# Optimization experiments

Measured on AMD Instinct MI355X. Metric: run time of the kernel, lower is better.

The kernel has to match this reference:

```python
import jax, jax.numpy as jnp
import numpy as np

H = 2048      # hidden_dim
OUT = 8       # output_dim
DICT = 50000  # dict_len (DND capacity)
FDIM = 6      # function_dim
RDIM = 1      # rule_dim
IN = FDIM + RDIM + OUT + 1  # input_dim = 16
NG = 5        # N_GATES
EPS = 1e-8


def setup_inputs() -> dict:
    key = jax.random.key(0)
    ks = jax.random.split(key, 16)
    f = lambda i, shape, s=1.0: jax.random.normal(ks[i], shape, jnp.float32) * s
    return {
        "x_t": f(0, (1, IN)),
        "h": f(1, (1, 1, H), 0.1),
        "c": f(2, (1, 1, H), 0.1),
        "W_i2h": f(3, ((NG + 1) * H, IN), 0.05),
        "b_i2h": jnp.zeros(((NG + 1) * H,), jnp.float32),
        "W_h2h": f(4, ((NG + 1) * H, H), 0.02),
        "b_h2h": jnp.zeros(((NG + 1) * H,), jnp.float32),
        "f_keys": f(5, (DICT, FDIM)),
        "f_vals": f(6, (DICT, H), 0.1),
        "r_keys": f(7, (DICT, RDIM)),
        "r_vals": f(8, (DICT, H), 0.1),
        "W_ih": f(9, (H, H), 0.02),
        "b_ih": jnp.zeros((H,), jnp.float32),
        "W_actor": f(10, (OUT, H), 0.02),
        "b_actor": jnp.zeros((OUT,), jnp.float32),
        "W_critic": f(11, (1, H), 0.02),
        "b_critic": jnp.zeros((1,), jnp.float32),
        "write_idx": 12345,
    }


def _dnd_read(q, keys, vals):
    # cosine similarity between query q [d] and all keys [N, d], softmax policy,
    # weighted sum over stored values [N, H] -> [H]
    qn = q / (jnp.linalg.norm(q) + EPS)
    kn = keys / (jnp.linalg.norm(keys, axis=1, keepdims=True) + EPS)
    sim = kn @ qn                      # [N]
    w = jax.nn.softmax(sim)            # [N]
    return w @ vals                    # [H]


def reference(x_t, h, c, W_i2h, b_i2h, W_h2h, b_h2h,
              f_keys, f_vals, r_keys, r_vals,
              W_ih, b_ih, W_actor, b_actor, W_critic, b_critic,
              write_idx):
    h2 = h.reshape(1, H)
    c2 = c.reshape(1, H)

    # fused gate preactivations: [1, 6H]
    preact = x_t @ W_i2h.T + b_i2h + h2 @ W_h2h.T + b_h2h
    gates = jax.nn.sigmoid(preact[:, :NG * H])
    f_t = gates[:, 0 * H:1 * H]
    i_t = gates[:, 1 * H:2 * H]
    o_t = gates[:, 2 * H:3 * H]
    fun_t = gates[:, 3 * H:4 * H]
    rul_t = gates[:, 4 * H:5 * H]
    c_new = jnp.tanh(preact[:, NG * H:])

    c_t = f_t * c2 + i_t * c_new

    # DND content-addressable reads (cosine sim + softmax over memory slots)
    q_f = x_t[0, :FDIM]
    q_r = x_t[0, FDIM:FDIM + RDIM]
    memfun_t = jnp.tanh(_dnd_read(q_f, f_keys, f_vals))  # [H]
    memrul_t = jnp.tanh(_dnd_read(q_r, r_keys, r_vals))  # [H]

    c_t = c_t + fun_t * memfun_t + rul_t * memrul_t
    h_t = o_t * jnp.tanh(c_t)

    # memory write (no-grad in original): function half / rule half of c_t
    c_ft = jax.lax.stop_gradient(c_t[0].at[H // 2:].set(0.0))
    c_rt = jax.lax.stop_gradient(c_t[0].at[:H // 2].set(0.0))
    new_f_keys = f_keys.at[write_idx].set(q_f)
    new_f_vals = f_vals.at[write_idx].set(c_ft)
    new_r_keys = r_keys.at[write_idx].set(q_r)
    new_r_vals = r_vals.at[write_idx].set(c_rt)

    # A2C head: shared relu layer, actor softmax, critic scalar
    ha = jax.nn.relu(h_t @ W_ih.T + b_ih)
    pi_a_t = jax.nn.softmax(ha @ W_actor.T + b_actor, axis=-1)  # [1, OUT]
    v_t = ha @ W_critic.T + b_critic                            # [1, 1]

    h_out = h_t.reshape(1, 1, H)
    c_out = c_t.reshape(1, 1, H)
    return (pi_a_t, v_t, h_out, c_out,
            new_f_keys, new_f_vals, new_r_keys, new_r_vals)
```

## Files before the change

### kernel.cpp

```cpp
#include <hip/hip_runtime.h>
#include <math.h>

#define H        2048
#define HD       12288
#define DICT     50000
#define FDIM     6
#define RDIM     1
#define IN_DIM   16
#define EPS_F    1e-8f

#define OFF_PI   ((size_t)0)
#define OFF_V    ((size_t)8)
#define OFF_H    ((size_t)9)
#define OFF_C    ((size_t)2057)
#define OFF_FK   ((size_t)4105)
#define OFF_FV   ((size_t)304105)
#define OFF_RK   ((size_t)102704105)
#define OFF_RV   ((size_t)102754105)

#define R_CHUNK      125
#define NBLK_DICT    (DICT / R_CHUNK)
#define NBLK_VALS    (2 * NBLK_DICT)
#define NBLK_PREACT  (HD / 8)
#define NBLK_TOTAL   (NBLK_VALS + NBLK_PREACT)

typedef float f4v __attribute__((ext_vector_type(4)));

__device__ __forceinline__ float sigf(float v) { return 1.0f / (1.0f + expf(-v)); }

__global__ void k_zero(float* __restrict__ p, int n) {
    int i = blockIdx.x * 256 + threadIdx.x;
    if (i < n) p[i] = 0.0f;
}

__global__ __launch_bounds__(512) void k_mega(
    const float* __restrict__ f_keys, const float* __restrict__ r_keys,
    const float* __restrict__ f_vals, const float* __restrict__ r_vals,
    const float* __restrict__ x,
    const float* __restrict__ W_h2h, const float* __restrict__ W_i2h,
    const float* __restrict__ b_h2h, const float* __restrict__ b_i2h,
    const float* __restrict__ h,
    float* __restrict__ out_fv, float* __restrict__ out_rv,
    float* __restrict__ out_fk, float* __restrict__ out_rk,
    float* __restrict__ memfun, float* __restrict__ memrul,
    float* __restrict__ sums, float* __restrict__ preact)
{
    const int b   = blockIdx.x;
    const int tid = threadIdx.x;

    if (b >= NBLK_VALS) {
        const int row  = (b - NBLK_VALS) * 8 + (tid >> 6);
        const int lane = tid & 63;
        const float4* Wv = (const float4*)(W_h2h + (size_t)row * H);
        const float4* hv = (const float4*)h;
        float acc = 0.0f;
#pragma unroll
        for (int k = 0; k < 8; ++k) {
            float4 w4 = Wv[lane + (k << 6)];
            float4 h4 = hv[lane + (k << 6)];
            acc += w4.x * h4.x + w4.y * h4.y + w4.z * h4.z + w4.w * h4.w;
        }
        if (lane < IN_DIM) acc += W_i2h[(size_t)row * IN_DIM + lane] * x[lane];
#pragma unroll
        for (int off = 32; off > 0; off >>= 1) acc += __shfl_down(acc, off);
        if (lane == 0) preact[row] = acc + b_h2h[row] + b_i2h[row];
        return;
    }

    __shared__ float wl[R_CHUNK];
    const int  dict = (b >= NBLK_DICT) ? 1 : 0;
    const int  row0 = (dict ? b - NBLK_DICT : b) * R_CHUNK;

    const float* vals = dict ? r_vals : f_vals;
    float*       outv = dict ? out_rv : out_fv;
    float*       mem  = dict ? memrul : memfun;

    if (!dict) {
        for (int i = tid; i < R_CHUNK * FDIM; i += 512)
            out_fk[(size_t)row0 * FDIM + i] = f_keys[(size_t)row0 * FDIM + i];
    } else if (tid < R_CHUNK) {
        out_rk[row0 + tid] = r_keys[row0 + tid];
    }

    if (tid < R_CHUNK) {
        const int row = row0 + tid;
        float e;
        if (!dict) {
            float qn[FDIM]; float qs = 0.0f;
#pragma unroll
            for (int d = 0; d < FDIM; ++d) { float q = x[d]; qn[d] = q; qs += q * q; }
            const float qi = 1.0f / (sqrtf(qs) + EPS_F);
            float ks = 0.0f, dot = 0.0f;
#pragma unroll
            for (int d = 0; d < FDIM; ++d) {
                float kv = f_keys[(size_t)row * FDIM + d];
                ks += kv * kv; dot += kv * qn[d];
            }
            e = expf((dot * qi) / (sqrtf(ks) + EPS_F));
        } else {
            float q  = x[FDIM];
            float kv = r_keys[row];
            e = expf((kv * (q / (fabsf(q) + EPS_F))) / (fabsf(kv) + EPS_F));
        }
        wl[tid] = e;
    }
    __syncthreads();
    if (tid == 0) {
        float s = 0.0f;
        for (int i = 0; i < R_CHUNK; ++i) s += wl[i];
        atomicAdd(&sums[dict], s);
    }

    const f4v* vv = (const f4v*)vals;
    float a0 = 0.f, a1 = 0.f, a2 = 0.f, a3 = 0.f;
    size_t base = (size_t)row0 * 512 + tid;
    for (int i0 = 0; i0 < R_CHUNK; i0 += 5) {
        f4v v0 = __builtin_nontemporal_load(&vv[base]);
        f4v v1 = __builtin_nontemporal_load(&vv[base +  512]);
        f4v v2 = __builtin_nontemporal_load(&vv[base + 1024]);
        f4v v3 = __builtin_nontemporal_load(&vv[base + 1536]);
        f4v v4 = __builtin_nontemporal_load(&vv[base + 2048]);
        const float w0 = wl[i0], w1 = wl[i0+1], w2 = wl[i0+2], w3 = wl[i0+3], w4 = wl[i0+4];
        a0 += w0*v0.x + w1*v1.x + w2*v2.x + w3*v3.x + w4*v4.x;
        a1 += w0*v0.y + w1*v1.y + w2*v2.y + w3*v3.y + w4*v4.y;
        a2 += w0*v0.z + w1*v1.z + w2*v2.z + w3*v3.z + w4*v4.z;
        a3 += w0*v0.w + w1*v1.w + w2*v2.w + w3*v3.w + w4*v4.w;
        float* o0 = outv + (base        ) * 4;
        float* o1 = outv + (base +  512 ) * 4;
        float* o2 = outv + (base + 1024 ) * 4;
        float* o3 = outv + (base + 1536 ) * 4;
        float* o4 = outv + (base + 2048 ) * 4;
        __builtin_nontemporal_store(v0.x, o0+0); __builtin_nontemporal_store(v0.y, o0+1);
        __builtin_nontemporal_store(v0.z, o0+2); __builtin_nontemporal_store(v0.w, o0+3);
        __builtin_nontemporal_store(v1.x, o1+0); __builtin_nontemporal_store(v1.y, o1+1);
        __builtin_nontemporal_store(v1.z, o1+2); __builtin_nontemporal_store(v1.w, o1+3);
        __builtin_nontemporal_store(v2.x, o2+0); __builtin_nontemporal_store(v2.y, o2+1);
        __builtin_nontemporal_store(v2.z, o2+2); __builtin_nontemporal_store(v2.w, o2+3);
        __builtin_nontemporal_store(v3.x, o3+0); __builtin_nontemporal_store(v3.y, o3+1);
        __builtin_nontemporal_store(v3.z, o3+2); __builtin_nontemporal_store(v3.w, o3+3);
        __builtin_nontemporal_store(v4.x, o4+0); __builtin_nontemporal_store(v4.y, o4+1);
        __builtin_nontemporal_store(v4.z, o4+2); __builtin_nontemporal_store(v4.w, o4+3);
        base += 5 * 512;
    }
    const int c = tid * 4;
    atomicAdd(&mem[c + 0], a0);
    atomicAdd(&mem[c + 1], a1);
    atomicAdd(&mem[c + 2], a2);
    atomicAdd(&mem[c + 3], a3);
}

__global__ __launch_bounds__(256) void k_combine(
    const float* __restrict__ preact, const float* __restrict__ c_in,
    const float* __restrict__ memfun, const float* __restrict__ memrul,
    const float* __restrict__ sums,
    const float* __restrict__ x, const int* __restrict__ widx_p,
    float* __restrict__ out, float* __restrict__ ht_ws)
{
    const int j = blockIdx.x * 256 + threadIdx.x;
    if (j >= H) return;
    const int widx = *widx_p;
    const float invf = 1.0f / sums[0];
    const float invr = 1.0f / sums[1];

    float f_t   = sigf(preact[0 * H + j]);
    float i_t   = sigf(preact[1 * H + j]);
    float o_t   = sigf(preact[2 * H + j]);
    float fun_t = sigf(preact[3 * H + j]);
    float rul_t = sigf(preact[4 * H + j]);
    float c_new = tanhf(preact[5 * H + j]);

    float ct = f_t * c_in[j] + i_t * c_new
             + fun_t * tanhf(memfun[j] * invf) + rul_t * tanhf(memrul[j] * invr);
    float ht = o_t * tanhf(ct);

    out[OFF_H + j] = ht;
    out[OFF_C + j] = ct;
    ht_ws[j] = ht;

    out[OFF_FV + (size_t)widx * H + j] = (j < H / 2) ? ct : 0.0f;
    out[OFF_RV + (size_t)widx * H + j] = (j < H / 2) ? 0.0f : ct;
    if (j < FDIM)  out[OFF_FK + (size_t)widx * FDIM + j] = x[j];
    if (j == FDIM) out[OFF_RK + (size_t)widx] = x[FDIM];
}

__global__ __launch_bounds__(256) void k_hidden(
    const float* __restrict__ W_ih, const float* __restrict__ b_ih,
    const float* __restrict__ ht, float* __restrict__ ha)
{
    int gid  = blockIdx.x * blockDim.x + threadIdx.x;
    int row  = gid >> 6;
    int lane = threadIdx.x & 63;
    if (row >= H) return;
    const float4* Wv = (const float4*)(W_ih + (size_t)row * H);
    const float4* hv = (const float4*)ht;
    float acc = 0.0f;
#pragma unroll
    for (int k = 0; k < 8; ++k) {
        float4 w4 = Wv[lane + (k << 6)];
        float4 h4 = hv[lane + (k << 6)];
        acc += w4.x * h4.x + w4.y * h4.y + w4.z * h4.z + w4.w * h4.w;
    }
#pragma unroll
    for (int off = 32; off > 0; off >>= 1) acc += __shfl_down(acc, off);
    if (lane == 0) ha[row] = fmaxf(acc + b_ih[row], 0.0f);
}

__global__ __launch_bounds__(256) void k_heads(
    const float* __restrict__ W_actor, const float* __restrict__ b_actor,
    const float* __restrict__ W_critic, const float* __restrict__ b_critic,
    const float* __restrict__ ha, float* __restrict__ out)
{
    __shared__ float red[4];
    __shared__ float logits[9];
    const int tid = threadIdx.x;

    for (int o = 0; o < 9; ++o) {
        const float* row = (o < 8) ? (W_actor + (size_t)o * H) : W_critic;
        float acc = 0.0f;
        for (int k = tid; k < H; k += 256) acc += row[k] * ha[k];
#pragma unroll
        for (int off = 32; off > 0; off >>= 1) acc += __shfl_down(acc, off);
        if ((tid & 63) == 0) red[tid >> 6] = acc;
        __syncthreads();
        if (tid == 0)
            logits[o] = red[0] + red[1] + red[2] + red[3] + ((o < 8) ? b_actor[o] : b_critic[0]);
        __syncthreads();
    }
    if (tid == 0) {
        float m = logits[0];
        for (int o = 1; o < 8; ++o) m = fmaxf(m, logits[o]);
        float e[8], s = 0.0f;
        for (int o = 0; o < 8; ++o) { e[o] = expf(logits[o] - m); s += e[o]; }
        for (int o = 0; o < 8; ++o) out[OFF_PI + o] = e[o] / s;
        out[OFF_V] = logits[8];
    }
}

extern "C" void kernel_launch(void* const* d_in, const int* in_sizes, int n_in,
                              void* d_out, int out_size, void* d_ws, size_t ws_size,
                              hipStream_t stream)
{
    const float* x        = (const float*)d_in[0];
    const float* h        = (const float*)d_in[1];
    const float* c        = (const float*)d_in[2];
    const float* W_i2h    = (const float*)d_in[3];
    const float* b_i2h    = (const float*)d_in[4];
    const float* W_h2h    = (const float*)d_in[5];
    const float* b_h2h    = (const float*)d_in[6];
    const float* f_keys   = (const float*)d_in[7];
    const float* f_vals   = (const float*)d_in[8];
    const float* r_keys   = (const float*)d_in[9];
    const float* r_vals   = (const float*)d_in[10];
    const float* W_ih     = (const float*)d_in[11];
    const float* b_ih     = (const float*)d_in[12];
    const float* W_actor  = (const float*)d_in[13];
    const float* b_actor  = (const float*)d_in[14];
    const float* W_critic = (const float*)d_in[15];
    const float* b_critic = (const float*)d_in[16];
    const int*   widx     = (const int*)d_in[17];

    float* out = (float*)d_out;
    float* ws  = (float*)d_ws;

    float* preact = ws;
    float* memfun = ws + 12288;
    float* memrul = ws + 14336;
    float* sums   = ws + 16384;
    float* ht_ws  = ws + 16388;
    float* ha     = ws + 18436;

    k_zero<<<17, 256, 0, stream>>>(memfun, 2 * H + 2);

    k_mega<<<NBLK_TOTAL, 512, 0, stream>>>(
        f_keys, r_keys, f_vals, r_vals, x,
        W_h2h, W_i2h, b_h2h, b_i2h, h,
        out + OFF_FV, out + OFF_RV, out + OFF_FK, out + OFF_RK,
        memfun, memrul, sums, preact);

    k_combine<<<H / 256, 256, 0, stream>>>(preact, c, memfun, memrul, sums, x, widx, out, ht_ws);

    k_hidden<<<H / 4, 256, 0, stream>>>(W_ih, b_ih, ht_ws, ha);
    k_heads<<<1, 256, 0, stream>>>(W_actor, b_actor, W_critic, b_critic, ha, out);
}
```

Before: 454.4 us.

## Realign value-copy stores with lane shuffles and split heads into parallel blocks

The output value tables start at odd float offsets, so the old per-float nontemporal stores were scalar and misaligned. The copy loop now shifts each row by three floats using cross-lane shuffles, so most stores become aligned 16-byte vector stores, with edge cases for lane 63 and the row ends. The single-block actor/critic head is split into a 9-block dot-product kernel plus a tiny softmax kernel. The split adds a kernel launch and an extra reload at wavefront boundaries in exchange for wider stores and parallel head reductions.

```diff
diff --git a/kernel.cpp b/kernel.cpp
--- a/kernel.cpp
+++ b/kernel.cpp
@@ -112,35 +112,34 @@
     }
 
     const f4v* vv = (const f4v*)vals;
+    const int lane = tid & 63;
     float a0 = 0.f, a1 = 0.f, a2 = 0.f, a3 = 0.f;
-    size_t base = (size_t)row0 * 512 + tid;
-    for (int i0 = 0; i0 < R_CHUNK; i0 += 5) {
-        f4v v0 = __builtin_nontemporal_load(&vv[base]);
-        f4v v1 = __builtin_nontemporal_load(&vv[base +  512]);
-        f4v v2 = __builtin_nontemporal_load(&vv[base + 1024]);
-        f4v v3 = __builtin_nontemporal_load(&vv[base + 1536]);
-        f4v v4 = __builtin_nontemporal_load(&vv[base + 2048]);
-        const float w0 = wl[i0], w1 = wl[i0+1], w2 = wl[i0+2], w3 = wl[i0+3], w4 = wl[i0+4];
-        a0 += w0*v0.x + w1*v1.x + w2*v2.x + w3*v3.x + w4*v4.x;
-        a1 += w0*v0.y + w1*v1.y + w2*v2.y + w3*v3.y + w4*v4.y;
-        a2 += w0*v0.z + w1*v1.z + w2*v2.z + w3*v3.z + w4*v4.z;
-        a3 += w0*v0.w + w1*v1.w + w2*v2.w + w3*v3.w + w4*v4.w;
-        float* o0 = outv + (base        ) * 4;
-        float* o1 = outv + (base +  512 ) * 4;
-        float* o2 = outv + (base + 1024 ) * 4;
-        float* o3 = outv + (base + 1536 ) * 4;
-        float* o4 = outv + (base + 2048 ) * 4;
-        __builtin_nontemporal_store(v0.x, o0+0); __builtin_nontemporal_store(v0.y, o0+1);
-        __builtin_nontemporal_store(v0.z, o0+2); __builtin_nontemporal_store(v0.w, o0+3);
-        __builtin_nontemporal_store(v1.x, o1+0); __builtin_nontemporal_store(v1.y, o1+1);
-        __builtin_nontemporal_store(v1.z, o1+2); __builtin_nontemporal_store(v1.w, o1+3);
-        __builtin_nontemporal_store(v2.x, o2+0); __builtin_nontemporal_store(v2.y, o2+1);
-        __builtin_nontemporal_store(v2.z, o2+2); __builtin_nontemporal_store(v2.w, o2+3);
-        __builtin_nontemporal_store(v3.x, o3+0); __builtin_nontemporal_store(v3.y, o3+1);
-        __builtin_nontemporal_store(v3.z, o3+2); __builtin_nontemporal_store(v3.w, o3+3);
-        __builtin_nontemporal_store(v4.x, o4+0); __builtin_nontemporal_store(v4.y, o4+1);
-        __builtin_nontemporal_store(v4.z, o4+2); __builtin_nontemporal_store(v4.w, o4+3);
-        base += 5 * 512;
+#pragma unroll 4
+    for (int i = 0; i < R_CHUNK; ++i) {
+        const size_t idx = (size_t)(row0 + i) * 512 + tid;
+        f4v v = __builtin_nontemporal_load(&vv[idx]);
+        const float w = wl[i];
+        a0 += w * v.x; a1 += w * v.y; a2 += w * v.z; a3 += w * v.w;
+
+        float nx = __shfl_down(v.x, 1);
+        float ny = __shfl_down(v.y, 1);
+        float nz = __shfl_down(v.z, 1);
+        if (lane == 63 && tid != 511) {
+            f4v e = vv[idx + 1];
+            nx = e.x; ny = e.y; nz = e.z;
+        }
+        float* orow = outv + (size_t)(row0 + i) * 2048;
+        if (tid < 511) {
+            f4v s; s.x = v.w; s.y = nx; s.z = ny; s.w = nz;
+            __builtin_nontemporal_store(s, (f4v*)(orow + 3) + tid);
+        } else {
+            __builtin_nontemporal_store(v.w, orow + 2047);
+        }
+        if (tid == 0) {
+            __builtin_nontemporal_store(v.x, orow + 0);
+            __builtin_nontemporal_store(v.y, orow + 1);
+            __builtin_nontemporal_store(v.z, orow + 2);
+        }
     }
     const int c = tid * 4;
     atomicAdd(&mem[c + 0], a0);
@@ -205,28 +204,37 @@
     if (lane == 0) ha[row] = fmaxf(acc + b_ih[row], 0.0f);
 }
 
-__global__ __launch_bounds__(256) void k_heads(
+__global__ __launch_bounds__(256) void k_heads1(
     const float* __restrict__ W_actor, const float* __restrict__ b_actor,
     const float* __restrict__ W_critic, const float* __restrict__ b_critic,
-    const float* __restrict__ ha, float* __restrict__ out)
+    const float* __restrict__ ha, float* __restrict__ logits)
 {
     __shared__ float red[4];
-    __shared__ float logits[9];
+    const int o   = blockIdx.x;
     const int tid = threadIdx.x;
-
-    for (int o = 0; o < 9; ++o) {
-        const float* row = (o < 8) ? (W_actor + (size_t)o * H) : W_critic;
-        float acc = 0.0f;
-        for (int k = tid; k < H; k += 256) acc += row[k] * ha[k];
-#pragma unroll
-        for (int off = 32; off > 0; off >>= 1) acc += __shfl_down(acc, off);
-        if ((tid & 63) == 0) red[tid >> 6] = acc;
-        __syncthreads();
-        if (tid == 0)
-            logits[o] = red[0] + red[1] + red[2] + red[3] + ((o < 8) ? b_actor[o] : b_critic[0]);
-        __syncthreads();
-    }
-    if (tid == 0) {
+    const float* row = (o < 8) ? (W_actor + (size_t)o * H) : W_critic;
+    const float4* rv = (const float4*)row;
+    const float4* hv = (const float4*)ha;
+    float acc = 0.0f;
+#pragma unroll
+    for (int k = 0; k < 2; ++k) {
+        int idx = tid + (k << 8);
+        float4 w4 = rv[idx];
+        float4 h4 = hv[idx];
+        acc += w4.x * h4.x + w4.y * h4.y + w4.z * h4.z + w4.w * h4.w;
+    }
+#pragma unroll
+    for (int off = 32; off > 0; off >>= 1) acc += __shfl_down(acc, off);
+    if ((tid & 63) == 0) red[tid >> 6] = acc;
+    __syncthreads();
+    if (tid == 0)
+        logits[o] = red[0] + red[1] + red[2] + red[3] + ((o < 8) ? b_actor[o] : b_critic[0]);
+}
+
+__global__ __launch_bounds__(64) void k_heads2(
+    const float* __restrict__ logits, float* __restrict__ out)
+{
+    if (threadIdx.x == 0) {
         float m = logits[0];
         for (int o = 1; o < 8; ++o) m = fmaxf(m, logits[o]);
         float e[8], s = 0.0f;
@@ -268,6 +276,7 @@
     float* sums   = ws + 16384;
     float* ht_ws  = ws + 16388;
     float* ha     = ws + 18436;
+    float* logits = ws + 20484;
 
     k_zero<<<17, 256, 0, stream>>>(memfun, 2 * H + 2);
 
@@ -280,5 +289,6 @@
     k_combine<<<H / 256, 256, 0, stream>>>(preact, c, memfun, memrul, sums, x, widx, out, ht_ws);
 
     k_hidden<<<H / 4, 256, 0, stream>>>(W_ih, b_ih, ht_ws, ha);
-    k_heads<<<1, 256, 0, stream>>>(W_actor, b_actor, W_critic, b_critic, ha, out);
-}
+    k_heads1<<<9, 256, 0, stream>>>(W_actor, b_actor, W_critic, b_critic, ha, logits);
+    k_heads2<<<1, 64, 0, stream>>>(logits, out);
+}
```

Result: slower. 1.007 ms (+121.7%).
